# Kernel optimization log

Measured on AMD Instinct MI355X. Metric: run time of the kernel, lower is better.

## Reference

```python
import jax, jax.numpy as jnp
import numpy as np

TAU = 2.0  # membrane time constant from init_kwargs


def setup_inputs() -> dict:
    key = jax.random.key(0)
    # [T, B, N] multi-step input (store_v_seq=True implies multi-step mode)
    x = jax.random.normal(key, (1024, 16, 2048), dtype=jnp.float32)
    return {"x": x}


def reference(x):
    # LIFNode with decay_input=True, v_reset=0.0:
    #   v_t = v_{t-1} + (x_t - v_{t-1}) / tau
    # v_threshold=1e9 means no spikes ever fire, so the module is a pure
    # leaky integrator (EMA with alpha = 1/tau); output = v_seq.
    inv_tau = jnp.asarray(1.0 / TAU, dtype=x.dtype)

    def step(v, xt):
        v = v + (xt - v) * inv_tau
        return v, v

    v0 = jnp.zeros(x.shape[1:], dtype=x.dtype)
    _, v_seq = jax.lax.scan(step, v0, x)  # [T, B, N]
    return v_seq
```

## Files before the change

### kernel.cpp

```cpp
#include <hip/hip_runtime.h>


constexpr int T    = 1024;
constexpr int E4   = 8192;
constexpr int L    = 32;
constexpr int C    = T / L;
constexpr int WARM = 12;

__global__ __launch_bounds__(256) void lif_chunked(const float4* __restrict__ x,
                                                   float4* __restrict__ out) {
    const int gid = blockIdx.x * 256 + threadIdx.x;
    const int g = gid & (E4 - 1);
    const int c = gid >> 13;

    const int t0 = c * L;
    float4 v = make_float4(0.f, 0.f, 0.f, 0.f);

    if (c > 0) {
        const float4* p = x + (size_t)(t0 - WARM) * E4 + g;
        #pragma unroll
        for (int k = 0; k < WARM; ++k) {
            float4 xv = p[(size_t)k * E4];
            v.x = fmaf(0.5f, xv.x - v.x, v.x);
            v.y = fmaf(0.5f, xv.y - v.y, v.y);
            v.z = fmaf(0.5f, xv.z - v.z, v.z);
            v.w = fmaf(0.5f, xv.w - v.w, v.w);
        }
    }

    const float4* p = x   + (size_t)t0 * E4 + g;
    float4*       q = out + (size_t)t0 * E4 + g;
    #pragma unroll
    for (int k = 0; k < L; ++k) {
        float4 xv = p[(size_t)k * E4];
        v.x = fmaf(0.5f, xv.x - v.x, v.x);
        v.y = fmaf(0.5f, xv.y - v.y, v.y);
        v.z = fmaf(0.5f, xv.z - v.z, v.z);
        v.w = fmaf(0.5f, xv.w - v.w, v.w);
        q[(size_t)k * E4] = v;
    }
}

extern "C" void kernel_launch(void* const* d_in, const int* in_sizes, int n_in,
                              void* d_out, int out_size, void* d_ws, size_t ws_size,
                              hipStream_t stream) {
    const float4* x = (const float4*)d_in[0];
    float4* out = (float4*)d_out;
    const int total_threads = E4 * C;
    const int blocks = total_threads / 256;
    lif_chunked<<<blocks, 256, 0, stream>>>(x, out);
}
```

Before: 55.47 us.

## Double the chunk length, software-pipeline loads, and use nontemporal stores

Doubles the time-chunk length to 64 and raises the warm-up to 16 steps, which cuts redundant warm-up reads. The main loop now prefetches the next four timesteps into registers while the current four are computed, and outputs are written with nontemporal stores to keep them out of the cache. The cost is half as many threads (16 chunks x 8192), so less parallelism to hide memory latency. Warm-up truncation error shrinks slightly at WARM=16.

```diff
diff --git a/kernel.cpp b/kernel.cpp
--- a/kernel.cpp
+++ b/kernel.cpp
@@ -1,52 +1,66 @@
 #include <hip/hip_runtime.h>
 
 
+typedef float v4f __attribute__((ext_vector_type(4)));
+
 constexpr int T    = 1024;
 constexpr int E4   = 8192;
-constexpr int L    = 32;
+constexpr int L    = 64;
 constexpr int C    = T / L;
-constexpr int WARM = 12;
+constexpr int WARM = 16;
 
-__global__ __launch_bounds__(256) void lif_chunked(const float4* __restrict__ x,
-                                                   float4* __restrict__ out) {
+__device__ __forceinline__ void step(v4f& v, const v4f xv) {
+    v = v + (xv - v) * 0.5f;
+}
+
+__global__ __launch_bounds__(256) void lif_pipe(const v4f* __restrict__ x,
+                                                v4f* __restrict__ out) {
     const int gid = blockIdx.x * 256 + threadIdx.x;
     const int g = gid & (E4 - 1);
     const int c = gid >> 13;
 
     const int t0 = c * L;
-    float4 v = make_float4(0.f, 0.f, 0.f, 0.f);
+    v4f v = (v4f)(0.f);
 
     if (c > 0) {
-        const float4* p = x + (size_t)(t0 - WARM) * E4 + g;
+        const v4f* p = x + (size_t)(t0 - WARM) * E4 + g;
         #pragma unroll
         for (int k = 0; k < WARM; ++k) {
-            float4 xv = p[(size_t)k * E4];
-            v.x = fmaf(0.5f, xv.x - v.x, v.x);
-            v.y = fmaf(0.5f, xv.y - v.y, v.y);
-            v.z = fmaf(0.5f, xv.z - v.z, v.z);
-            v.w = fmaf(0.5f, xv.w - v.w, v.w);
+            step(v, p[(size_t)k * E4]);
         }
     }
 
-    const float4* p = x   + (size_t)t0 * E4 + g;
-    float4*       q = out + (size_t)t0 * E4 + g;
-    #pragma unroll
-    for (int k = 0; k < L; ++k) {
-        float4 xv = p[(size_t)k * E4];
-        v.x = fmaf(0.5f, xv.x - v.x, v.x);
-        v.y = fmaf(0.5f, xv.y - v.y, v.y);
-        v.z = fmaf(0.5f, xv.z - v.z, v.z);
-        v.w = fmaf(0.5f, xv.w - v.w, v.w);
-        q[(size_t)k * E4] = v;
+    const v4f* p = x   + (size_t)t0 * E4 + g;
+    v4f*       q = out + (size_t)t0 * E4 + g;
+
+    v4f b0 = p[0];
+    v4f b1 = p[(size_t)1 * E4];
+    v4f b2 = p[(size_t)2 * E4];
+    v4f b3 = p[(size_t)3 * E4];
+
+    for (int k = 0; k < L - 4; k += 4) {
+        v4f n0 = p[(size_t)(k + 4) * E4];
+        v4f n1 = p[(size_t)(k + 5) * E4];
+        v4f n2 = p[(size_t)(k + 6) * E4];
+        v4f n3 = p[(size_t)(k + 7) * E4];
+        step(v, b0); __builtin_nontemporal_store(v, q + (size_t)(k + 0) * E4);
+        step(v, b1); __builtin_nontemporal_store(v, q + (size_t)(k + 1) * E4);
+        step(v, b2); __builtin_nontemporal_store(v, q + (size_t)(k + 2) * E4);
+        step(v, b3); __builtin_nontemporal_store(v, q + (size_t)(k + 3) * E4);
+        b0 = n0; b1 = n1; b2 = n2; b3 = n3;
     }
+    step(v, b0); __builtin_nontemporal_store(v, q + (size_t)(L - 4) * E4);
+    step(v, b1); __builtin_nontemporal_store(v, q + (size_t)(L - 3) * E4);
+    step(v, b2); __builtin_nontemporal_store(v, q + (size_t)(L - 2) * E4);
+    step(v, b3); __builtin_nontemporal_store(v, q + (size_t)(L - 1) * E4);
 }
 
 extern "C" void kernel_launch(void* const* d_in, const int* in_sizes, int n_in,
                               void* d_out, int out_size, void* d_ws, size_t ws_size,
                               hipStream_t stream) {
-    const float4* x = (const float4*)d_in[0];
-    float4* out = (float4*)d_out;
+    const v4f* x = (const v4f*)d_in[0];
+    v4f* out = (v4f*)d_out;
     const int total_threads = E4 * C;
     const int blocks = total_threads / 256;
-    lif_chunked<<<blocks, 256, 0, stream>>>(x, out);
+    lif_pipe<<<blocks, 256, 0, stream>>>(x, out);
 }
```

New measurement: 52.60 us. -5.2%, faster.
